# Performance work log

Measured on AMD Instinct MI355X. Metric: run time of the kernel, lower is better.

## Reference

```python
import jax, jax.numpy as jnp
import numpy as np

N = 50000
E = 800000
IN_FEAT = 128
HEADS = 2
HEAD_DIM = 64  # hidden_feat // num_heads for 'concat'
HIDDEN = HEADS * HEAD_DIM
N_CLASSES = 16
NEG_SLOPE = 0.2
BN_EPS = 1e-5


def setup_inputs() -> dict:
    key = jax.random.key(0)
    ks = jax.random.split(key, 20)
    s = 0.1  # weight scale for numerical sanity
    return {
        "x": jax.random.normal(ks[0], (N, IN_FEAT), jnp.float32),
        "src0": jax.random.randint(ks[1], (E,), 0, N, jnp.int32),
        "dst0": jax.random.randint(ks[2], (E,), 0, N, jnp.int32),
        "ew0": jax.random.uniform(ks[3], (E,), jnp.float32),
        "src1": jax.random.randint(ks[4], (E,), 0, N, jnp.int32),
        "dst1": jax.random.randint(ks[5], (E,), 0, N, jnp.int32),
        "ew1": jax.random.uniform(ks[6], (E,), jnp.float32),
        "fc_w0": jax.random.normal(ks[7], (HIDDEN, IN_FEAT), jnp.float32) * s,
        "bias0": jnp.zeros((HIDDEN,), jnp.float32),
        "attn_l0": jax.random.normal(ks[8], (HEADS, HEAD_DIM), jnp.float32) * s,
        "attn_r0": jax.random.normal(ks[9], (HEADS, HEAD_DIM), jnp.float32) * s,
        "fc_w1": jax.random.normal(ks[10], (HIDDEN, IN_FEAT), jnp.float32) * s,
        "bias1": jnp.zeros((HIDDEN,), jnp.float32),
        "attn_l1": jax.random.normal(ks[11], (HEADS, HEAD_DIM), jnp.float32) * s,
        "attn_r1": jax.random.normal(ks[12], (HEADS, HEAD_DIM), jnp.float32) * s,
        "skip_w": jax.random.normal(ks[13], (HIDDEN, IN_FEAT), jnp.float32) * s,
        "skip_b": jnp.zeros((HIDDEN,), jnp.float32),
        "bn_gamma": jnp.ones((HIDDEN,), jnp.float32),
        "bn_beta": jnp.zeros((HIDDEN,), jnp.float32),
        "clf_w": jax.random.normal(ks[14], (N_CLASSES, HIDDEN), jnp.float32) * s,
        "clf_b": jnp.zeros((N_CLASSES,), jnp.float32),
    }


def _weighted_gat(x, src, dst, ew, fc_w, bias, attn_l, attn_r):
    # DGL GATConv with per-edge weight scaling of attention.
    f = (x @ fc_w.T).reshape(N, HEADS, HEAD_DIM)          # [N,H,D]
    el = jnp.sum(f * attn_l, axis=-1)                      # [N,H]
    er = jnp.sum(f * attn_r, axis=-1)                      # [N,H]
    e = jax.nn.leaky_relu(el[src] + er[dst], NEG_SLOPE)    # [E,H]
    # edge softmax over incoming edges of each dst, numerically stable
    m = jax.ops.segment_max(e, dst, num_segments=N)        # [N,H]
    ex = jnp.exp(e - m[dst])
    den = jax.ops.segment_sum(ex, dst, num_segments=N)     # [N,H]
    alpha = ex / den[dst]                                  # [E,H]
    alpha = alpha * ew[:, None]                            # edge-weight scaling
    msg = alpha[..., None] * f[src]                        # [E,H,D]
    out = jax.ops.segment_sum(msg, dst, num_segments=N)    # [N,H,D]
    return out + bias.reshape(1, HEADS, HEAD_DIM)


def reference(x, src0, dst0, ew0, src1, dst1, ew1,
              fc_w0, bias0, attn_l0, attn_r0,
              fc_w1, bias1, attn_l1, attn_r1,
              skip_w, skip_b, bn_gamma, bn_beta, clf_w, clf_b):
    # HeteroGraphConv with aggregate='sum': sum per-relation GAT outputs
    h2 = _weighted_gat(x, src0, dst0, ew0, fc_w0, bias0, attn_l0, attn_r0) \
       + _weighted_gat(x, src1, dst1, ew1, fc_w1, bias1, attn_l1, attn_r1)
    # multihead 'concat' aggregate with relu: flatten heads
    h2 = jax.nn.relu(h2).reshape(N, HIDDEN)
    # linear skip + residual add (dropout is identity at eval)
    h = (x @ skip_w.T + skip_b) + h2
    # classifier: BatchNorm1d (batch stats) -> ReLU -> Linear
    mu = jnp.mean(h, axis=0)
    var = jnp.mean((h - mu) ** 2, axis=0)
    hn = (h - mu) * jax.lax.rsqrt(var + BN_EPS) * bn_gamma + bn_beta
    logits = jax.nn.relu(hn) @ clf_w.T + clf_b
    return logits
```

## Files before the change

kernel.cpp:

```cpp
#include <hip/hip_runtime.h>
#include <hip/hip_bf16.h>

#define N_NODES 50000
#define N_EDGES 800000
#define HID 128
#define NEG_SLOPE 0.2f
#define BN_EPS 1e-5f

#define NBLK 256
#define BINSZ 512
#define BINSH 9
#define NBINS 98

typedef __bf16 v8bf __attribute__((ext_vector_type(8)));
typedef float v4f __attribute__((ext_vector_type(4)));

__device__ __forceinline__ float leaky(float v) {
    return (v > 0.f) ? v : v * NEG_SLOPE;
}
__device__ __forceinline__ unsigned int f2bu(float f) {
    __hip_bfloat16 b = __float2bfloat16(f);
    return (unsigned int)*reinterpret_cast<unsigned short*>(&b);
}
__device__ __forceinline__ unsigned int pack2bf(float lo, float hi) {
    return f2bu(lo) | (f2bu(hi) << 16);
}

__global__ __launch_bounds__(256) void k_prepw(const float* __restrict__ w0,
                                               const float* __restrict__ w1,
                                               const float* __restrict__ wsk,
                                               unsigned short* __restrict__ wb) {
    const int WQ = 128 * 128 / 4;
    int q = blockIdx.x * 256 + threadIdx.x;
    if (q >= 3 * WQ) return;
    int mat = q >> 12;
    int rem = q & 4095;
    const float* W = (mat == 0) ? w0 : (mat == 1) ? w1 : wsk;
    float4 v = ((const float4*)W)[rem];
    ushort4 o;
    o.x = (unsigned short)f2bu(v.x);
    o.y = (unsigned short)f2bu(v.y);
    o.z = (unsigned short)f2bu(v.z);
    o.w = (unsigned short)f2bu(v.w);
    *(ushort4*)(wb + (size_t)mat * 16384 + rem * 4) = o;
}

__global__ __launch_bounds__(256) void k_bincount(const int* __restrict__ dst0,
                                                  const int* __restrict__ dst1,
                                                  int* __restrict__ bincnt) {
    int rel = blockIdx.y;
    const int* dst = rel ? dst1 : dst0;
    __shared__ int cnt[NBINS];
    for (int i = threadIdx.x; i < NBINS; i += 256) cnt[i] = 0;
    __syncthreads();
    const int CH = (N_EDGES + NBLK - 1) / NBLK;
    int b0 = blockIdx.x * CH;
    int b1 = min(N_EDGES, b0 + CH);
    for (int e = b0 + threadIdx.x; e < b1; e += 256)
        atomicAdd(&cnt[dst[e] >> BINSH], 1);
    __syncthreads();
    for (int i = threadIdx.x; i < NBINS; i += 256)
        bincnt[rel * NBINS * NBLK + i * NBLK + blockIdx.x] = cnt[i];
}

__global__ __launch_bounds__(1024) void k_binscan(int* __restrict__ bincnt) {
    int* a = bincnt + blockIdx.x * NBINS * NBLK;
    const int TOT = NBINS * NBLK;
    const int CH = (TOT + 1023) / 1024;
    int tid = threadIdx.x;
    int base = tid * CH;
    int lv[CH];
    int sum = 0;
    for (int i = 0; i < CH; i++) {
        int idx = base + i;
        int v = (idx < TOT) ? a[idx] : 0;
        lv[i] = sum;
        sum += v;
    }
    __shared__ int ls[1024];
    ls[tid] = sum;
    __syncthreads();
    for (int ofs = 1; ofs < 1024; ofs <<= 1) {
        int v = (tid >= ofs) ? ls[tid - ofs] : 0;
        __syncthreads();
        ls[tid] += v;
        __syncthreads();
    }
    int pre = tid ? ls[tid - 1] : 0;
    for (int i = 0; i < CH; i++) {
        int idx = base + i;
        if (idx < TOT) a[idx] = pre + lv[i];
    }
}

__global__ __launch_bounds__(256) void k_binscatter(const int* __restrict__ dst0,
                                                    const int* __restrict__ dst1,
                                                    const int* __restrict__ src0,
                                                    const int* __restrict__ src1,
                                                    const float* __restrict__ ew0,
                                                    const float* __restrict__ ew1,
                                                    const int* __restrict__ bincnt,
                                                    int2* __restrict__ pairs0,
                                                    int2* __restrict__ pairs1) {
    int rel = blockIdx.y;
    const int* dst = rel ? dst1 : dst0;
    const int* src = rel ? src1 : src0;
    const float* ew = rel ? ew1 : ew0;
    int2* pairs = rel ? pairs1 : pairs0;
    __shared__ int cur[NBINS];
    for (int i = threadIdx.x; i < NBINS; i += 256)
        cur[i] = bincnt[rel * NBINS * NBLK + i * NBLK + blockIdx.x];
    __syncthreads();
    const int CH = (N_EDGES + NBLK - 1) / NBLK;
    int b0 = blockIdx.x * CH;
    int b1 = min(N_EDGES, b0 + CH);
    for (int e = b0 + threadIdx.x; e < b1; e += 256) {
        int d = dst[e];
        int pos = atomicAdd(&cur[d >> BINSH], 1);
        unsigned int packed = (unsigned int)(d & (BINSZ - 1)) |
                              ((unsigned int)src[e] << BINSH);
        pairs[pos] = make_int2((int)packed, __float_as_int(ew[e]));
    }
}

__global__ __launch_bounds__(256) void k_csr(const int* __restrict__ bincnt,
                                             const int2* __restrict__ pairs0,
                                             const int2* __restrict__ pairs1,
                                             const float* __restrict__ el0,
                                             const float* __restrict__ er0,
                                             const float* __restrict__ el1,
                                             const float* __restrict__ er1,
                                             int* __restrict__ offs0,
                                             int* __restrict__ offs1,
                                             int2* __restrict__ rec0,
                                             int2* __restrict__ rec1,
                                             float2* __restrict__ den20,
                                             float2* __restrict__ den21) {
    int rel = blockIdx.y;
    const int2* pairs = rel ? pairs1 : pairs0;
    const float* el = rel ? el1 : el0;
    const float* er = rel ? er1 : er0;
    int* offs = rel ? offs1 : offs0;
    int2* rec = rel ? rec1 : rec0;
    float2* den2 = rel ? den21 : den20;
    int bin = blockIdx.x;
    int tid = threadIdx.x;
    const int* bc = bincnt + rel * NBINS * NBLK;
    int pbase = bc[bin * NBLK];
    int pend = (bin < NBINS - 1) ? bc[(bin + 1) * NBLK] : N_EDGES;
    int n0 = bin << BINSH;
    int nn = min(N_NODES - n0, BINSZ);

    __shared__ int s_deg[BINSZ];
    __shared__ int s_ts[256];
    __shared__ float sden[BINSZ * 2];
    for (int i = tid; i < BINSZ; i += 256) s_deg[i] = 0;
    for (int i = tid; i < BINSZ * 2; i += 256) sden[i] = 0.f;
    __syncthreads();
    for (int p = pbase + tid; p < pend; p += 256)
        atomicAdd(&s_deg[((unsigned int)pairs[p].x) & (BINSZ - 1)], 1);
    __syncthreads();

    int d0 = s_deg[tid * 2], d1 = s_deg[tid * 2 + 1];
    s_ts[tid] = d0 + d1;
    __syncthreads();
    for (int ofs = 1; ofs < 256; ofs <<= 1) {
        int v = (tid >= ofs) ? s_ts[tid - ofs] : 0;
        __syncthreads();
        s_ts[tid] += v;
        __syncthreads();
    }
    int pre = tid ? s_ts[tid - 1] : 0;
    s_deg[tid * 2] = pbase + pre;
    s_deg[tid * 2 + 1] = pbase + pre + d0;
    __syncthreads();

    for (int l = tid; l < nn; l += 256) offs[n0 + l] = s_deg[l];
    if (bin == NBINS - 1 && tid == 0) offs[N_NODES] = N_EDGES;
    __syncthreads();

    for (int p = pbase + tid; p < pend; p += 256) {
        int2 pr = pairs[p];
        unsigned int u = (unsigned int)pr.x;
        int dl = (int)(u & (BINSZ - 1));
        int s = (int)(u >> BINSH);
        int pos = atomicAdd(&s_deg[dl], 1);
        float2 ev = *(const float2*)(el + 2 * s);
        float2 rv = *(const float2*)(er + 2 * (n0 + dl));
        float x0 = expf(leaky(ev.x + rv.x));
        float x1 = expf(leaky(ev.y + rv.y));
        atomicAdd(&sden[dl * 2], x0);
        atomicAdd(&sden[dl * 2 + 1], x1);
        float ew = __int_as_float(pr.y);
        rec[pos] = make_int2(s << 8, (int)pack2bf(x0 * ew, x1 * ew));
    }
    __syncthreads();
    for (int l = tid; l < nn; l += 256)
        den2[n0 + l] = make_float2(sden[l * 2], sden[l * 2 + 1]);
}

__global__ __launch_bounds__(256) void k_gemm_mfma(
    const float* __restrict__ x, const unsigned short* __restrict__ wb,
    const float* __restrict__ skip_b,
    const float* __restrict__ al0, const float* __restrict__ ar0,
    const float* __restrict__ al1, const float* __restrict__ ar1,
    unsigned short* __restrict__ fb0, unsigned short* __restrict__ fb1,
    float* __restrict__ el0, float* __restrict__ er0,
    float* __restrict__ el1, float* __restrict__ er1,
    float* __restrict__ hs) {
    __shared__ unsigned short As[64][128];
    __shared__ unsigned short Bs[64][128];
    int tid = threadIdx.x;
    int m0 = blockIdx.x * 64;

#pragma unroll
    for (int i = 0; i < 4; i++) {
        int idx = tid * 4 + i;
        int row = idx >> 4, seg = idx & 15;
        int gr = m0 + row;
        uint4 o = make_uint4(0, 0, 0, 0);
        if (gr < N_NODES) {
            const float* p = x + (size_t)gr * HID + seg * 8;
            float4 p0 = *(const float4*)p;
            float4 p1 = *(const float4*)(p + 4);
            o.x = pack2bf(p0.x, p0.y);
            o.y = pack2bf(p0.z, p0.w);
            o.z = pack2bf(p1.x, p1.y);
            o.w = pack2bf(p1.z, p1.w);
        }
        *(uint4*)(&As[row][(seg ^ (row & 7)) * 8]) = o;
    }
    __syncthreads();

    int w = tid >> 6, l = tid & 63;
    int lr = l & 15, lg = l >> 4;
    int node = m0 + w * 16 + lr;
    bool valid = node < N_NODES;
    int arow = w * 16 + lr;
    v8bf afrag[4];
#pragma unroll
    for (int kb = 0; kb < 4; kb++)
        afrag[kb] = *(v8bf*)(&As[arow][((kb * 4 + lg) ^ (arow & 7)) * 8]);

    for (int s = 0; s < 6; s++) {
        int mat = s >> 1;
        int j0 = (s & 1) * 64;
        const unsigned short* wmat = wb + (size_t)mat * 16384 + j0 * HID;
        __syncthreads();
#pragma unroll
        for (int i = 0; i < 4; i++) {
            int idx = tid * 4 + i;
            int row = idx >> 4, seg = idx & 15;
            uint4 wv = *(const uint4*)(wmat + row * HID + seg * 8);
            *(uint4*)(&Bs[row][(seg ^ (row & 7)) * 8]) = wv;
        }
        __syncthreads();

        v4f acc[4] = {};
#pragma unroll
        for (int nt = 0; nt < 4; nt++) {
            int brow = nt * 16 + lr;
#pragma unroll
            for (int kb = 0; kb < 4; kb++) {
                v8bf bfrag =
                    *(v8bf*)(&Bs[brow][((kb * 4 + lg) ^ (brow & 7)) * 8]);
                acc[nt] = __builtin_amdgcn_mfma_f32_16x16x32_bf16(
                    bfrag, afrag[kb], acc[nt], 0, 0, 0);
            }
        }

        if (mat < 2) {
            int h = s & 1;
            const float* al = mat ? al1 : al0;
            const float* ar = mat ? ar1 : ar0;
            float* elp = mat ? el1 : el0;
            float* erp = mat ? er1 : er0;
            unsigned short* fbp = mat ? fb1 : fb0;
            float elv = 0.f, erv = 0.f;
#pragma unroll
            for (int nt = 0; nt < 4; nt++) {
                int c0 = j0 + nt * 16 + lg * 4;
                float4 av = *(const float4*)(al + c0);
                float4 rv = *(const float4*)(ar + c0);
                elv += acc[nt][0] * av.x + acc[nt][1] * av.y +
                       acc[nt][2] * av.z + acc[nt][3] * av.w;
                erv += acc[nt][0] * rv.x + acc[nt][1] * rv.y +
                       acc[nt][2] * rv.z + acc[nt][3] * rv.w;
            }
            elv += __shfl_xor(elv, 16);
            elv += __shfl_xor(elv, 32);
            erv += __shfl_xor(erv, 16);
            erv += __shfl_xor(erv, 32);
            if (valid) {
#pragma unroll
                for (int nt = 0; nt < 4; nt++) {
                    uint2 o;
                    o.x = pack2bf(acc[nt][0], acc[nt][1]);
                    o.y = pack2bf(acc[nt][2], acc[nt][3]);
                    *(uint2*)(fbp + (size_t)node * HID + j0 + nt * 16 + lg * 4) = o;
                }
                if (lg == 0) {
                    elp[node * 2 + h] = elv;
                    erp[node * 2 + h] = erv;
                }
            }
        } else if (valid) {
#pragma unroll
            for (int nt = 0; nt < 4; nt++) {
                int c0 = j0 + nt * 16 + lg * 4;
                float4 sb = *(const float4*)(skip_b + c0);
                float4 o;
                o.x = acc[nt][0] + sb.x;
                o.y = acc[nt][1] + sb.y;
                o.z = acc[nt][2] + sb.z;
                o.w = acc[nt][3] + sb.w;
                *(float4*)(hs + (size_t)node * HID + c0) = o;
            }
        }
    }
}

__device__ __forceinline__ void agg_rel2(const int* __restrict__ offs,
                                         const int2* __restrict__ rec,
                                         const float2* __restrict__ den2,
                                         const unsigned char* __restrict__ fbb,
                                         int n, int lane, int sub,
                                         int hh, float* a) {
    int b = offs[n];
    int e_end = offs[n + 1];
    int deg = e_end - b;
    if (deg <= 0) return;
    float2 dn = den2[n];
    float inv0 = 1.f / dn.x, inv1 = 1.f / dn.y;

    int nchunk = (deg + 63) >> 6;
    for (int ch = 0; ch < nchunk; ch++) {
        int p = b + (ch << 6) + lane;
        int s = 0;
        unsigned int wpk = 0;
        if (p < e_end) {
            int2 r = rec[p];
            s = r.x;
            wpk = (unsigned int)r.y;
        }
        unsigned int pk = pack2bf(__uint_as_float(wpk << 16) * inv0,
                                  __uint_as_float(wpk & 0xffff0000u) * inv1);
        int cnt = deg - (ch << 6);
        if (cnt > 64) cnt = 64;
        int ng = (cnt + 3) >> 2;
#pragma unroll 2
        for (int g = 0; g < ng; g++) {
            int sl = (g << 2) + sub;
            int sj = __shfl(s, sl);
            unsigned int pkj = (unsigned int)__shfl((int)pk, sl);
            float aj = __uint_as_float(hh ? (pkj & 0xffff0000u) : (pkj << 16));
            uint4 fv = *(const uint4*)(fbb + sj);
            a[0] += aj * __uint_as_float(fv.x << 16);
            a[1] += aj * __uint_as_float(fv.x & 0xffff0000u);
            a[2] += aj * __uint_as_float(fv.y << 16);
            a[3] += aj * __uint_as_float(fv.y & 0xffff0000u);
            a[4] += aj * __uint_as_float(fv.z << 16);
            a[5] += aj * __uint_as_float(fv.z & 0xffff0000u);
            a[6] += aj * __uint_as_float(fv.w << 16);
            a[7] += aj * __uint_as_float(fv.w & 0xffff0000u);
        }
    }
}

__global__ __launch_bounds__(256) void k_aggregate(
    const int* __restrict__ offs0, const int2* __restrict__ rec0,
    const float2* __restrict__ den20, const unsigned short* __restrict__ fb0,
    const int* __restrict__ offs1, const int2* __restrict__ rec1,
    const float2* __restrict__ den21, const unsigned short* __restrict__ fb1,
    const float* __restrict__ bias0, const float* __restrict__ bias1,
    float* __restrict__ h) {
    int wave = threadIdx.x >> 6, lane = threadIdx.x & 63;
    int n = blockIdx.x * 4 + wave;
    if (n >= N_NODES) return;
    int cb = lane & 15;
    int sub = lane >> 4;
    int hh = cb >> 3;
    float a[8] = {0.f, 0.f, 0.f, 0.f, 0.f, 0.f, 0.f, 0.f};
    const unsigned char* fbb0 = (const unsigned char*)fb0 + cb * 16;
    const unsigned char* fbb1 = (const unsigned char*)fb1 + cb * 16;
    agg_rel2(offs0, rec0, den20, fbb0, n, lane, sub, hh, a);
    agg_rel2(offs1, rec1, den21, fbb1, n, lane, sub, hh, a);
#pragma unroll
    for (int j = 0; j < 8; j++) {
        a[j] += __shfl_xor(a[j], 16);
        a[j] += __shfl_xor(a[j], 32);
    }
    if (sub == 0) {
        size_t base = (size_t)n * HID + cb * 8;
        float4 v0 = *(const float4*)(h + base);
        float4 v1 = *(const float4*)(h + base + 4);
        int c0 = cb * 8;
        float4 o0, o1;
        o0.x = v0.x + fmaxf(a[0] + bias0[c0 + 0] + bias1[c0 + 0], 0.f);
        o0.y = v0.y + fmaxf(a[1] + bias0[c0 + 1] + bias1[c0 + 1], 0.f);
        o0.z = v0.z + fmaxf(a[2] + bias0[c0 + 2] + bias1[c0 + 2], 0.f);
        o0.w = v0.w + fmaxf(a[3] + bias0[c0 + 3] + bias1[c0 + 3], 0.f);
        o1.x = v1.x + fmaxf(a[4] + bias0[c0 + 4] + bias1[c0 + 4], 0.f);
        o1.y = v1.y + fmaxf(a[5] + bias0[c0 + 5] + bias1[c0 + 5], 0.f);
        o1.z = v1.z + fmaxf(a[6] + bias0[c0 + 6] + bias1[c0 + 6], 0.f);
        o1.w = v1.w + fmaxf(a[7] + bias0[c0 + 7] + bias1[c0 + 7], 0.f);
        *(float4*)(h + base) = o0;
        *(float4*)(h + base + 4) = o1;
    }
}

__global__ __launch_bounds__(256) void k_bnstats(const float* __restrict__ h,
                                                 double* __restrict__ psum,
                                                 double* __restrict__ psumsq) {
    int tid = threadIdx.x;
    const float4* h4 = (const float4*)h;
    double s[4] = {0.0, 0.0, 0.0, 0.0};
    double q[4] = {0.0, 0.0, 0.0, 0.0};
    const int totalv = N_NODES * HID / 4;
    const int stride = 512 * 256;
    for (int i = blockIdx.x * 256 + tid; i < totalv; i += stride) {
        float4 v = h4[i];
        s[0] += v.x; q[0] += (double)v.x * v.x;
        s[1] += v.y; q[1] += (double)v.y * v.y;
        s[2] += v.z; q[2] += (double)v.z * v.z;
        s[3] += v.w; q[3] += (double)v.w * v.w;
    }
    __shared__ double ls[256][4], lq[256][4];
#pragma unroll
    for (int j = 0; j < 4; j++) {
        ls[tid][j] = s[j];
        lq[tid][j] = q[j];
    }
    __syncthreads();
    if (tid < 32) {
#pragma unroll
        for (int j = 0; j < 4; j++) {
            double ss = 0.0, qq = 0.0;
            for (int t = tid; t < 256; t += 32) {
                ss += ls[t][j];
                qq += lq[t][j];
            }
            psum[blockIdx.x * 128 + tid * 4 + j] = ss;
            psumsq[blockIdx.x * 128 + tid * 4 + j] = qq;
        }
    }
}

__global__ void k_bn_finalize(const double* __restrict__ psum,
                              const double* __restrict__ psumsq,
                              const float* __restrict__ gamma,
                              const float* __restrict__ beta,
                              float* __restrict__ ss) {
    int c = threadIdx.x;
    double s = 0.0, q = 0.0;
    for (int b = 0; b < 512; b++) {
        s += psum[b * 128 + c];
        q += psumsq[b * 128 + c];
    }
    double mu = s / N_NODES;
    double var = q / N_NODES - mu * mu;
    float sc = gamma[c] * (float)(1.0 / sqrt(var + (double)BN_EPS));
    ss[c] = sc;
    ss[128 + c] = beta[c] - (float)mu * sc;
}

__global__ __launch_bounds__(256) void k_classify(const float* __restrict__ h,
                                                  const float* __restrict__ ss,
                                                  const float* __restrict__ clf_w,
                                                  const float* __restrict__ clf_b,
                                                  float* __restrict__ out) {
    int w = threadIdx.x >> 6, l = threadIdx.x & 63;
    int lr = l & 15, lg = l >> 4;
    int n0 = (blockIdx.x * 4 + w) * 16;
    if (n0 >= N_NODES) return;

    v8bf afrag[4], bfrag[4];
#pragma unroll
    for (int kb = 0; kb < 4; kb++) {
        int k0 = kb * 32 + lg * 8;
        const float* bp = clf_w + lr * HID + k0;
        float4 b0 = *(const float4*)bp;
        float4 b1 = *(const float4*)(bp + 4);
        bfrag[kb][0] = (__bf16)b0.x; bfrag[kb][1] = (__bf16)b0.y;
        bfrag[kb][2] = (__bf16)b0.z; bfrag[kb][3] = (__bf16)b0.w;
        bfrag[kb][4] = (__bf16)b1.x; bfrag[kb][5] = (__bf16)b1.y;
        bfrag[kb][6] = (__bf16)b1.z; bfrag[kb][7] = (__bf16)b1.w;
        const float* ap = h + (size_t)(n0 + lr) * HID + k0;
        float4 a0 = *(const float4*)ap;
        float4 a1 = *(const float4*)(ap + 4);
        float4 sc0 = *(const float4*)(ss + k0);
        float4 sc1 = *(const float4*)(ss + k0 + 4);
        float4 sh0 = *(const float4*)(ss + 128 + k0);
        float4 sh1 = *(const float4*)(ss + 128 + k0 + 4);
        afrag[kb][0] = (__bf16)fmaxf(a0.x * sc0.x + sh0.x, 0.f);
        afrag[kb][1] = (__bf16)fmaxf(a0.y * sc0.y + sh0.y, 0.f);
        afrag[kb][2] = (__bf16)fmaxf(a0.z * sc0.z + sh0.z, 0.f);
        afrag[kb][3] = (__bf16)fmaxf(a0.w * sc0.w + sh0.w, 0.f);
        afrag[kb][4] = (__bf16)fmaxf(a1.x * sc1.x + sh1.x, 0.f);
        afrag[kb][5] = (__bf16)fmaxf(a1.y * sc1.y + sh1.y, 0.f);
        afrag[kb][6] = (__bf16)fmaxf(a1.z * sc1.z + sh1.z, 0.f);
        afrag[kb][7] = (__bf16)fmaxf(a1.w * sc1.w + sh1.w, 0.f);
    }
    v4f acc = {};
#pragma unroll
    for (int kb = 0; kb < 4; kb++)
        acc = __builtin_amdgcn_mfma_f32_16x16x32_bf16(bfrag[kb], afrag[kb],
                                                      acc, 0, 0, 0);
    float4 cb = *(const float4*)(clf_b + lg * 4);
    float4 o;
    o.x = acc[0] + cb.x;
    o.y = acc[1] + cb.y;
    o.z = acc[2] + cb.z;
    o.w = acc[3] + cb.w;
    *(float4*)(out + (size_t)(n0 + lr) * 16 + lg * 4) = o;
}

extern "C" void kernel_launch(void* const* d_in, const int* in_sizes, int n_in,
                              void* d_out, int out_size, void* d_ws, size_t ws_size,
                              hipStream_t stream) {
    (void)in_sizes; (void)n_in; (void)out_size; (void)ws_size;
    const float* x      = (const float*)d_in[0];
    const int*   src0   = (const int*)d_in[1];
    const int*   dst0   = (const int*)d_in[2];
    const float* ew0    = (const float*)d_in[3];
    const int*   src1   = (const int*)d_in[4];
    const int*   dst1   = (const int*)d_in[5];
    const float* ew1    = (const float*)d_in[6];
    const float* fc_w0  = (const float*)d_in[7];
    const float* bias0  = (const float*)d_in[8];
    const float* al0    = (const float*)d_in[9];
    const float* ar0    = (const float*)d_in[10];
    const float* fc_w1  = (const float*)d_in[11];
    const float* bias1  = (const float*)d_in[12];
    const float* al1    = (const float*)d_in[13];
    const float* ar1    = (const float*)d_in[14];
    const float* skip_w = (const float*)d_in[15];
    const float* skip_b = (const float*)d_in[16];
    const float* gamma  = (const float*)d_in[17];
    const float* beta   = (const float*)d_in[18];
    const float* clf_w  = (const float*)d_in[19];
    const float* clf_b  = (const float*)d_in[20];
    float* out = (float*)d_out;

    char* wsp = (char*)d_ws;
    size_t off = 0;
    auto alloc = [&](size_t bytes) -> char* {
        char* p = wsp + off;
        off += (bytes + 255) & ~(size_t)255;
        return p;
    };
    unsigned short* wbf = (unsigned short*)alloc((size_t)3 * 16384 * 2);
    unsigned short* fb0 = (unsigned short*)alloc((size_t)N_NODES * HID * 2);
    unsigned short* fb1 = (unsigned short*)alloc((size_t)N_NODES * HID * 2);
    float*  hs     = (float*)alloc((size_t)N_NODES * HID * 4);
    float*  el0    = (float*)alloc((size_t)N_NODES * 2 * 4);
    float*  er0    = (float*)alloc((size_t)N_NODES * 2 * 4);
    float*  el1    = (float*)alloc((size_t)N_NODES * 2 * 4);
    float*  er1    = (float*)alloc((size_t)N_NODES * 2 * 4);
    int*    bincnt = (int*)alloc((size_t)2 * NBINS * NBLK * 4);
    int2*   pairs0 = (int2*)alloc((size_t)N_EDGES * 8);
    int2*   pairs1 = (int2*)alloc((size_t)N_EDGES * 8);
    int*    offs0  = (int*)alloc((size_t)(N_NODES + 1) * 4);
    int*    offs1  = (int*)alloc((size_t)(N_NODES + 1) * 4);
    int2*   rec0   = (int2*)alloc((size_t)N_EDGES * 8);
    int2*   rec1   = (int2*)alloc((size_t)N_EDGES * 8);
    float2* den20  = (float2*)alloc((size_t)N_NODES * 8);
    float2* den21  = (float2*)alloc((size_t)N_NODES * 8);
    double* psum   = (double*)alloc((size_t)512 * 128 * 8);
    double* psumsq = (double*)alloc((size_t)512 * 128 * 8);
    float*  ss     = (float*)alloc(256 * 4);

    k_prepw<<<48, 256, 0, stream>>>(fc_w0, fc_w1, skip_w, wbf);

    dim3 gbin(NBLK, 2);
    k_bincount<<<gbin, 256, 0, stream>>>(dst0, dst1, bincnt);
    k_binscan<<<2, 1024, 0, stream>>>(bincnt);
    k_binscatter<<<gbin, 256, 0, stream>>>(dst0, dst1, src0, src1, ew0, ew1,
                                           bincnt, pairs0, pairs1);

    k_gemm_mfma<<<(N_NODES + 63) / 64, 256, 0, stream>>>(
        x, wbf, skip_b, al0, ar0, al1, ar1,
        fb0, fb1, el0, er0, el1, er1, hs);

    dim3 gcsr(NBINS, 2);
    k_csr<<<gcsr, 256, 0, stream>>>(bincnt, pairs0, pairs1,
                                    el0, er0, el1, er1,
                                    offs0, offs1, rec0, rec1, den20, den21);

    k_aggregate<<<(N_NODES + 3) / 4, 256, 0, stream>>>(
        offs0, rec0, den20, fb0, offs1, rec1, den21, fb1, bias0, bias1, hs);

    k_bnstats<<<512, 256, 0, stream>>>(hs, psum, psumsq);
    k_bn_finalize<<<1, 128, 0, stream>>>(psum, psumsq, gamma, beta, ss);
    k_classify<<<(N_NODES + 63) / 64, 256, 0, stream>>>(
        hs, ss, clf_w, clf_b, out);
}
```

Measured before the change: 228.5 us.

## Merge weight prep with bin count, widen GEMM N-tile, unroll aggregation more

Fuses the weight-to-bf16 conversion kernel into the destination bin-count kernel, which removes one launch. The MFMA GEMM now processes all 128 output columns of each weight matrix per pass instead of two 64-column halves, so it needs fewer barriers and weight-tile loads. That costs a larger B shared tile (32KB) and more accumulator registers, which may reduce occupancy. The gather loop in aggregation is unrolled 4x instead of 2x to put more loads in flight.

```diff
diff --git a/kernel.cpp b/kernel.cpp
--- a/kernel.cpp
+++ b/kernel.cpp
@@ -26,41 +26,42 @@
     return f2bu(lo) | (f2bu(hi) << 16);
 }
 
-__global__ __launch_bounds__(256) void k_prepw(const float* __restrict__ w0,
-                                               const float* __restrict__ w1,
-                                               const float* __restrict__ wsk,
-                                               unsigned short* __restrict__ wb) {
-    const int WQ = 128 * 128 / 4;
-    int q = blockIdx.x * 256 + threadIdx.x;
-    if (q >= 3 * WQ) return;
-    int mat = q >> 12;
-    int rem = q & 4095;
-    const float* W = (mat == 0) ? w0 : (mat == 1) ? w1 : wsk;
-    float4 v = ((const float4*)W)[rem];
-    ushort4 o;
-    o.x = (unsigned short)f2bu(v.x);
-    o.y = (unsigned short)f2bu(v.y);
-    o.z = (unsigned short)f2bu(v.z);
-    o.w = (unsigned short)f2bu(v.w);
-    *(ushort4*)(wb + (size_t)mat * 16384 + rem * 4) = o;
-}
-
-__global__ __launch_bounds__(256) void k_bincount(const int* __restrict__ dst0,
-                                                  const int* __restrict__ dst1,
-                                                  int* __restrict__ bincnt) {
-    int rel = blockIdx.y;
-    const int* dst = rel ? dst1 : dst0;
-    __shared__ int cnt[NBINS];
-    for (int i = threadIdx.x; i < NBINS; i += 256) cnt[i] = 0;
-    __syncthreads();
-    const int CH = (N_EDGES + NBLK - 1) / NBLK;
-    int b0 = blockIdx.x * CH;
-    int b1 = min(N_EDGES, b0 + CH);
-    for (int e = b0 + threadIdx.x; e < b1; e += 256)
-        atomicAdd(&cnt[dst[e] >> BINSH], 1);
-    __syncthreads();
-    for (int i = threadIdx.x; i < NBINS; i += 256)
-        bincnt[rel * NBINS * NBLK + i * NBLK + blockIdx.x] = cnt[i];
+__global__ __launch_bounds__(256) void k_prep_count(
+    const float* __restrict__ w0, const float* __restrict__ w1,
+    const float* __restrict__ wsk, unsigned short* __restrict__ wb,
+    const int* __restrict__ dst0, const int* __restrict__ dst1,
+    int* __restrict__ bincnt) {
+    int bid = blockIdx.x;
+    if (bid < 2 * NBLK) {
+        int rel = bid / NBLK;
+        int blk = bid % NBLK;
+        const int* dst = rel ? dst1 : dst0;
+        __shared__ int cnt[NBINS];
+        for (int i = threadIdx.x; i < NBINS; i += 256) cnt[i] = 0;
+        __syncthreads();
+        const int CH = (N_EDGES + NBLK - 1) / NBLK;
+        int b0 = blk * CH;
+        int b1 = min(N_EDGES, b0 + CH);
+        for (int e = b0 + threadIdx.x; e < b1; e += 256)
+            atomicAdd(&cnt[dst[e] >> BINSH], 1);
+        __syncthreads();
+        for (int i = threadIdx.x; i < NBINS; i += 256)
+            bincnt[rel * NBINS * NBLK + i * NBLK + blk] = cnt[i];
+    } else {
+        const int WQ = 128 * 128 / 4;
+        int q = (bid - 2 * NBLK) * 256 + threadIdx.x;
+        if (q >= 3 * WQ) return;
+        int mat = q >> 12;
+        int rem = q & 4095;
+        const float* W = (mat == 0) ? w0 : (mat == 1) ? w1 : wsk;
+        float4 v = ((const float4*)W)[rem];
+        ushort4 o;
+        o.x = (unsigned short)f2bu(v.x);
+        o.y = (unsigned short)f2bu(v.y);
+        o.z = (unsigned short)f2bu(v.z);
+        o.w = (unsigned short)f2bu(v.w);
+        *(ushort4*)(wb + (size_t)mat * 16384 + rem * 4) = o;
+    }
 }
 
 __global__ __launch_bounds__(1024) void k_binscan(int* __restrict__ bincnt) {
@@ -209,7 +210,7 @@
     float* __restrict__ el1, float* __restrict__ er1,
     float* __restrict__ hs) {
     __shared__ unsigned short As[64][128];
-    __shared__ unsigned short Bs[64][128];
+    __shared__ unsigned short Bs[128][128];
     int tid = threadIdx.x;
     int m0 = blockIdx.x * 64;
 
@@ -242,23 +243,21 @@
     for (int kb = 0; kb < 4; kb++)
         afrag[kb] = *(v8bf*)(&As[arow][((kb * 4 + lg) ^ (arow & 7)) * 8]);
 
-    for (int s = 0; s < 6; s++) {
-        int mat = s >> 1;
-        int j0 = (s & 1) * 64;
-        const unsigned short* wmat = wb + (size_t)mat * 16384 + j0 * HID;
-        __syncthreads();
-#pragma unroll
-        for (int i = 0; i < 4; i++) {
-            int idx = tid * 4 + i;
+    for (int mat = 0; mat < 3; mat++) {
+        const unsigned short* wmat = wb + (size_t)mat * 16384;
+        __syncthreads();
+#pragma unroll
+        for (int i = 0; i < 8; i++) {
+            int idx = tid * 8 + i;
             int row = idx >> 4, seg = idx & 15;
             uint4 wv = *(const uint4*)(wmat + row * HID + seg * 8);
             *(uint4*)(&Bs[row][(seg ^ (row & 7)) * 8]) = wv;
         }
         __syncthreads();
 
-        v4f acc[4] = {};
-#pragma unroll
-        for (int nt = 0; nt < 4; nt++) {
+        v4f acc[8] = {};
+#pragma unroll
+        for (int nt = 0; nt < 8; nt++) {
             int brow = nt * 16 + lr;
 #pragma unroll
             for (int kb = 0; kb < 4; kb++) {
@@ -270,44 +269,51 @@
         }
 
         if (mat < 2) {
-            int h = s & 1;
             const float* al = mat ? al1 : al0;
             const float* ar = mat ? ar1 : ar0;
             float* elp = mat ? el1 : el0;
             float* erp = mat ? er1 : er0;
             unsigned short* fbp = mat ? fb1 : fb0;
-            float elv = 0.f, erv = 0.f;
-#pragma unroll
-            for (int nt = 0; nt < 4; nt++) {
-                int c0 = j0 + nt * 16 + lg * 4;
+            float elv0 = 0.f, erv0 = 0.f, elv1 = 0.f, erv1 = 0.f;
+#pragma unroll
+            for (int nt = 0; nt < 8; nt++) {
+                int c0 = nt * 16 + lg * 4;
                 float4 av = *(const float4*)(al + c0);
                 float4 rv = *(const float4*)(ar + c0);
-                elv += acc[nt][0] * av.x + acc[nt][1] * av.y +
-                       acc[nt][2] * av.z + acc[nt][3] * av.w;
-                erv += acc[nt][0] * rv.x + acc[nt][1] * rv.y +
-                       acc[nt][2] * rv.z + acc[nt][3] * rv.w;
+                float e = acc[nt][0] * av.x + acc[nt][1] * av.y +
+                          acc[nt][2] * av.z + acc[nt][3] * av.w;
+                float r = acc[nt][0] * rv.x + acc[nt][1] * rv.y +
+                          acc[nt][2] * rv.z + acc[nt][3] * rv.w;
+                if (nt < 4) { elv0 += e; erv0 += r; }
+                else        { elv1 += e; erv1 += r; }
             }
-            elv += __shfl_xor(elv, 16);
-            elv += __shfl_xor(elv, 32);
-            erv += __shfl_xor(erv, 16);
-            erv += __shfl_xor(erv, 32);
+            elv0 += __shfl_xor(elv0, 16);
+            elv0 += __shfl_xor(elv0, 32);
+            erv0 += __shfl_xor(erv0, 16);
+            erv0 += __shfl_xor(erv0, 32);
+            elv1 += __shfl_xor(elv1, 16);
+            elv1 += __shfl_xor(elv1, 32);
+            erv1 += __shfl_xor(erv1, 16);
+            erv1 += __shfl_xor(erv1, 32);
             if (valid) {
 #pragma unroll
-                for (int nt = 0; nt < 4; nt++) {
+                for (int nt = 0; nt < 8; nt++) {
                     uint2 o;
                     o.x = pack2bf(acc[nt][0], acc[nt][1]);
                     o.y = pack2bf(acc[nt][2], acc[nt][3]);
-                    *(uint2*)(fbp + (size_t)node * HID + j0 + nt * 16 + lg * 4) = o;
+                    *(uint2*)(fbp + (size_t)node * HID + nt * 16 + lg * 4) = o;
                 }
                 if (lg == 0) {
-                    elp[node * 2 + h] = elv;
-                    erp[node * 2 + h] = erv;
+                    elp[node * 2 + 0] = elv0;
+                    erp[node * 2 + 0] = erv0;
+                    elp[node * 2 + 1] = elv1;
+                    erp[node * 2 + 1] = erv1;
                 }
             }
         } else if (valid) {
 #pragma unroll
-            for (int nt = 0; nt < 4; nt++) {
-                int c0 = j0 + nt * 16 + lg * 4;
+            for (int nt = 0; nt < 8; nt++) {
+                int c0 = nt * 16 + lg * 4;
                 float4 sb = *(const float4*)(skip_b + c0);
                 float4 o;
                 o.x = acc[nt][0] + sb.x;
@@ -348,7 +354,7 @@
         int cnt = deg - (ch << 6);
         if (cnt > 64) cnt = 64;
         int ng = (cnt + 3) >> 2;
-#pragma unroll 2
+#pragma unroll 4
         for (int g = 0; g < ng; g++) {
             int sl = (g << 2) + sub;
             int sj = __shfl(s, sl);
@@ -570,11 +576,10 @@
     double* psumsq = (double*)alloc((size_t)512 * 128 * 8);
     float*  ss     = (float*)alloc(256 * 4);
 
-    k_prepw<<<48, 256, 0, stream>>>(fc_w0, fc_w1, skip_w, wbf);
-
+    k_prep_count<<<2 * NBLK + 48, 256, 0, stream>>>(fc_w0, fc_w1, skip_w, wbf,
+                                                    dst0, dst1, bincnt);
+    k_binscan<<<2, 1024, 0, stream>>>(bincnt);
     dim3 gbin(NBLK, 2);
-    k_bincount<<<gbin, 256, 0, stream>>>(dst0, dst1, bincnt);
-    k_binscan<<<2, 1024, 0, stream>>>(bincnt);
     k_binscatter<<<gbin, 256, 0, stream>>>(dst0, dst1, src0, src1, ew0, ew1,
                                            bincnt, pairs0, pairs1);
 
```

Result: no change. 232.6 us (+1.8%).
